# Kernel optimization log

Hardware: AMD Instinct MI355X
Metric: run time of the kernel (lower is better)

The kernel has to match this reference:

```python
import jax, jax.numpy as jnp
import numpy as np

N_NODES = 500000
N_EDGES = 16000000
IN_DIM = 17


def setup_inputs() -> dict:
    key = jax.random.key(0)
    k1, k2, k3, k4, k5, k6, k7 = jax.random.split(key, 7)
    x = jax.random.normal(k1, (N_NODES, IN_DIM), dtype=jnp.float32)
    edge_index = jax.random.randint(k2, (2, N_EDGES), 0, N_NODES, dtype=jnp.int64)
    edge_weight = jax.random.uniform(k3, (N_EDGES,), dtype=jnp.float32)
    # SAGEConv(17, 1): lin_l applied to aggregated neighbors (with bias),
    # lin_r applied to root features (no bias, PyG convention).
    s = 1.0 / np.sqrt(IN_DIM)
    w_l = jax.random.uniform(k4, (1, IN_DIM), minval=-s, maxval=s, dtype=jnp.float32)
    b_l = jax.random.uniform(k5, (1,), minval=-s, maxval=s, dtype=jnp.float32)
    w_r = jax.random.uniform(k6, (1, IN_DIM), minval=-s, maxval=s, dtype=jnp.float32)
    # out: Linear(1, 1)
    k8, k9 = jax.random.split(k7)
    w_o = jax.random.uniform(k8, (1, 1), minval=-1.0, maxval=1.0, dtype=jnp.float32)
    b_o = jax.random.uniform(k9, (1,), minval=-1.0, maxval=1.0, dtype=jnp.float32)
    return {"x": x, "edge_index": edge_index, "edge_weight": edge_weight,
            "w_l": w_l, "b_l": b_l, "w_r": w_r, "w_o": w_o, "b_o": b_o}


def reference(x, edge_index, edge_weight, w_l, b_l, w_r, w_o, b_o):
    # SAGEConv (mean aggregation). edge_weight is unused (faithful to PyG SAGEConv).
    # Project to out_dim=1 BEFORE aggregation (linearity makes this exact and
    # avoids materializing a [E,17] gathered buffer):
    #   lin_l(mean_j x_j) + b_l == mean_j (x_j @ W_l^T) + b_l
    src, dst = edge_index[0], edge_index[1]
    x_proj_l = x @ w_l.T                      # [N, 1]
    msg = x_proj_l[src, 0]                    # [E]  gathered source projections
    agg = jax.ops.segment_sum(msg, dst, num_segments=x.shape[0])          # [N]
    cnt = jax.ops.segment_sum(jnp.ones_like(msg), dst, num_segments=x.shape[0])
    mean = agg / jnp.maximum(cnt, 1.0)        # zero for isolated nodes
    h = mean[:, None] + b_l + x @ w_r.T       # [N, 1]  lin_l(aggr) + lin_r(x)
    h = jax.nn.elu(h)
    return h @ w_o.T + b_o                    # [N, 1]
```

## Files before the change

kernel.cpp:

```cpp
#include <hip/hip_runtime.h>
#include <hip/hip_bf16.h>
#include <math.h>

#define IN_DIM 17
#define NB 128
#define LOG_BN 12
#define BN 4096
#define K_SPLIT 16
#define CHUNK 8192
#define EPT 32
#define VAL_SCALE 4096.0f
#define FP_SCALE 268435456.0f
#define FP_INV   (1.0 / 268435456.0)

__global__ void node_proj_kernel(const float* __restrict__ x,
                                 const float* __restrict__ w_l,
                                 const float* __restrict__ w_r,
                                 float* __restrict__ p_l,
                                 float* __restrict__ p_r,
                                 int n_nodes) {
    int i = blockIdx.x * blockDim.x + threadIdx.x;
    if (i >= n_nodes) return;
    const float* row = x + (size_t)i * IN_DIM;
    float sl = 0.0f, sr = 0.0f;
#pragma unroll
    for (int k = 0; k < IN_DIM; ++k) {
        float v = row[k];
        sl = fmaf(v, w_l[k], sl);
        sr = fmaf(v, w_r[k], sr);
    }
    p_l[i] = sl;
    p_r[i] = sr;
}

__global__ __launch_bounds__(256, 4)
void sort_scatter_kernel(const int* __restrict__ src,
                         const int* __restrict__ dst,
                         const float* __restrict__ p_l,
                         unsigned* __restrict__ staging,
                         unsigned short* __restrict__ segtab,
                         int n_edges) {
    __shared__ unsigned hist[NB];
    __shared__ unsigned pos[NB];
    __shared__ unsigned sstart[NB + 1];
    __shared__ unsigned lbuf[CHUNK];

    const int tid = threadIdx.x;
    const int blk = blockIdx.x;
    const int e0 = blk * CHUNK;
    const int chunk_n = min(CHUNK, n_edges - e0);
    const int nvec = chunk_n >> 2;

    for (int t = tid; t < NB; t += 256) hist[t] = 0;
    __syncthreads();

    const uint4* dv = (const uint4*)(dst + e0);
    const uint4* sv = (const uint4*)(src + e0);
#pragma unroll
    for (int k = 0; k < EPT / 4; ++k) {
        int q = tid + k * 256;
        if (q < nvec) {
            uint4 d = dv[q];
            atomicAdd(&hist[d.x >> LOG_BN], 1u);
            atomicAdd(&hist[d.y >> LOG_BN], 1u);
            atomicAdd(&hist[d.z >> LOG_BN], 1u);
            atomicAdd(&hist[d.w >> LOG_BN], 1u);
        }
    }
    for (int i = (nvec << 2) + tid; i < chunk_n; i += 256)
        atomicAdd(&hist[(unsigned)dst[e0 + i] >> LOG_BN], 1u);
    __syncthreads();

    if (tid < 64) {
        unsigned c0 = hist[tid], c1 = hist[tid + 64];
        unsigned s0 = c0;
#pragma unroll
        for (int off = 1; off < 64; off <<= 1) {
            unsigned v = __shfl_up(s0, off);
            if (tid >= off) s0 += v;
        }
        unsigned tot0 = __shfl(s0, 63);
        unsigned s1 = c1;
#pragma unroll
        for (int off = 1; off < 64; off <<= 1) {
            unsigned v = __shfl_up(s1, off);
            if (tid >= off) s1 += v;
        }
        s1 += tot0;
        sstart[tid + 1] = s0;
        sstart[tid + 65] = s1;
        if (tid == 0) sstart[0] = 0;
        pos[tid] = (tid == 0) ? 0u : 0u;
    }
    __syncthreads();
    for (int t = tid; t < NB; t += 256) pos[t] = sstart[t];
    __syncthreads();

    for (int t = tid; t <= NB; t += 256)
        segtab[(size_t)blk * (NB + 2) + t] = (unsigned short)sstart[t];

#pragma unroll
    for (int k = 0; k < EPT / 4; ++k) {
        int q = tid + k * 256;
        if (q < nvec) {
            uint4 d = dv[q];
            uint4 s = sv[q];
            float pf[4] = {p_l[s.x], p_l[s.y], p_l[s.z], p_l[s.w]};
            unsigned dd[4] = {d.x, d.y, d.z, d.w};
#pragma unroll
            for (int u = 0; u < 4; ++u) {
                int fx = __float2int_rn(pf[u] * VAL_SCALE);
                fx = max(-32768, min(32767, fx));
                unsigned entry = ((unsigned)(fx & 0xFFFF) << 16) | (dd[u] & (BN - 1));
                unsigned b = dd[u] >> LOG_BN;
                unsigned p = atomicAdd(&pos[b], 1u);
                lbuf[p] = entry;
            }
        }
    }
    for (int i = (nvec << 2) + tid; i < chunk_n; i += 256) {
        unsigned s = (unsigned)src[e0 + i];
        unsigned d = (unsigned)dst[e0 + i];
        int fx = __float2int_rn(p_l[s] * VAL_SCALE);
        fx = max(-32768, min(32767, fx));
        unsigned entry = ((unsigned)(fx & 0xFFFF) << 16) | (d & (BN - 1));
        unsigned b = d >> LOG_BN;
        unsigned p = atomicAdd(&pos[b], 1u);
        lbuf[p] = entry;
    }
    __syncthreads();

    uint4* outp = (uint4*)(staging + (size_t)blk * CHUNK);
    const uint4* lp = (const uint4*)lbuf;
    int nv4 = (chunk_n + 3) >> 2;
    for (int q = tid; q < nv4; q += 256)
        outp[q] = lp[q];
}

__global__ __launch_bounds__(256, 8)
void reduce_kernel(const unsigned* __restrict__ staging,
                   const unsigned short* __restrict__ segtab,
                   unsigned* __restrict__ partials,
                   int nblk) {
    __shared__ unsigned lds_p[BN];
    const int tid = threadIdx.x;
    const int b = blockIdx.x / K_SPLIT;
    const int j = blockIdx.x % K_SPLIT;
    const int wave = tid >> 6, lane = tid & 63;

    for (int i = tid; i < BN; i += 256) lds_p[i] = 0u;
    __syncthreads();

    const int blk0 = (int)((long long)nblk * j / K_SPLIT);
    const int blk1 = (int)((long long)nblk * (j + 1) / K_SPLIT);

    int blk = blk0 + wave;
    unsigned s_nxt = 0, e_nxt = 0;
    if (blk < blk1) {
        const unsigned short* st = segtab + (size_t)blk * (NB + 2) + b;
        s_nxt = st[0];
        e_nxt = st[1];
    }
    while (blk < blk1) {
        unsigned s = s_nxt, e = e_nxt;
        const int nxt = blk + 4;
        if (nxt < blk1) {
            const unsigned short* st = segtab + (size_t)nxt * (NB + 2) + b;
            s_nxt = st[0];
            e_nxt = st[1];
        }
        const unsigned* sp = staging + (size_t)blk * CHUNK;
        for (unsigned i = s + lane; i < e; i += 64) {
            unsigned en = sp[i];
            int v = (int)(short)(en >> 16);
            atomicAdd(&lds_p[en & (BN - 1)], ((unsigned)v << 8) | 1u);
        }
        blk = nxt;
    }
    __syncthreads();
    size_t out_base = (size_t)blockIdx.x * BN;
    for (int i = tid; i < BN; i += 256)
        partials[out_base + i] = lds_p[i];
}

__global__ void finalize_kernel(const float* __restrict__ p_r,
                                const unsigned* __restrict__ partials,
                                const float* __restrict__ b_l,
                                const float* __restrict__ w_o,
                                const float* __restrict__ b_o,
                                float* __restrict__ out,
                                int n_nodes) {
    int i = blockIdx.x * blockDim.x + threadIdx.x;
    if (i >= n_nodes) return;
    int b = i >> LOG_BN;
    int loc = i & (BN - 1);
    int sum24 = 0, cnt = 0;
#pragma unroll
    for (int j = 0; j < K_SPLIT; ++j) {
        unsigned u = partials[((size_t)b * K_SPLIT + j) * BN + loc];
        sum24 += ((int)u) >> 8;
        cnt += (int)(u & 0xFFu);
    }
    float sum = (float)sum24 * (1.0f / VAL_SCALE);
    float mean = sum / fmaxf((float)cnt, 1.0f);
    float h = mean + b_l[0] + p_r[i];
    h = (h > 0.0f) ? h : expm1f(h);
    out[i] = fmaf(h, w_o[0], b_o[0]);
}

__global__ void edge_scatter_fb(const int* __restrict__ edge_index,
                                const float* __restrict__ p_l,
                                unsigned long long* __restrict__ bins,
                                int n_edges) {
    int e = blockIdx.x * blockDim.x + threadIdx.x;
    if (e >= n_edges) return;
    int s = edge_index[e];
    int d = edge_index[n_edges + e];
    float p = p_l[s];
    long long sfx = (long long)llrintf(p * FP_SCALE);
    unsigned long long delta = ((unsigned long long)sfx << 20) | 1ULL;
    atomicAdd(&bins[d], delta);
}

__global__ void finalize_fb(const float* __restrict__ p_r,
                            const unsigned long long* __restrict__ bins,
                            const float* __restrict__ b_l,
                            const float* __restrict__ w_o,
                            const float* __restrict__ b_o,
                            float* __restrict__ out,
                            int n_nodes) {
    int i = blockIdx.x * blockDim.x + threadIdx.x;
    if (i >= n_nodes) return;
    long long packed = (long long)bins[i];
    int cntv = (int)(packed & 0xFFFFFLL);
    long long sfx = packed >> 20;
    float sum = (float)((double)sfx * FP_INV);
    float mean = sum / fmaxf((float)cntv, 1.0f);
    float h = mean + b_l[0] + p_r[i];
    h = (h > 0.0f) ? h : expm1f(h);
    out[i] = fmaf(h, w_o[0], b_o[0]);
}

static inline size_t align_up(size_t v, size_t a) { return (v + a - 1) & ~(a - 1); }

extern "C" void kernel_launch(void* const* d_in, const int* in_sizes, int n_in,
                              void* d_out, int out_size, void* d_ws, size_t ws_size,
                              hipStream_t stream) {
    const float* x   = (const float*)d_in[0];
    const int*   ei  = (const int*)d_in[1];
    const float* w_l = (const float*)d_in[3];
    const float* b_l = (const float*)d_in[4];
    const float* w_r = (const float*)d_in[5];
    const float* w_o = (const float*)d_in[6];
    const float* b_o = (const float*)d_in[7];
    float* out = (float*)d_out;

    const int n_nodes = in_sizes[0] / IN_DIM;
    const int n_edges = in_sizes[2];
    const int* src = ei;
    const int* dst = ei + n_edges;
    const int nblk = (n_edges + CHUNK - 1) / CHUNK;

    char* ws = (char*)d_ws;
    size_t off = 0;
    size_t o_pl = off;      off = align_up(off + (size_t)n_nodes * 4, 256);
    size_t o_pr = off;      off = align_up(off + (size_t)n_nodes * 4, 256);
    size_t o_stage = off;   off = align_up(off + (size_t)nblk * CHUNK * 4, 256);
    size_t o_seg = off;     off = align_up(off + (size_t)nblk * (NB + 2) * 2, 256);
    size_t o_part = off;    off = align_up(off + (size_t)NB * K_SPLIT * BN * 4, 256);
    size_t need = off;

    float* p_l = (float*)(ws + o_pl);
    float* p_r = (float*)(ws + o_pr);

    const int B = 256;
    node_proj_kernel<<<(n_nodes + B - 1) / B, B, 0, stream>>>(x, w_l, w_r, p_l, p_r, n_nodes);

    if (ws_size >= need) {
        unsigned* staging       = (unsigned*)(ws + o_stage);
        unsigned short* segtab  = (unsigned short*)(ws + o_seg);
        unsigned* partials      = (unsigned*)(ws + o_part);

        sort_scatter_kernel<<<nblk, B, 0, stream>>>(src, dst, p_l, staging, segtab, n_edges);
        reduce_kernel<<<NB * K_SPLIT, B, 0, stream>>>(staging, segtab, partials, nblk);
        finalize_kernel<<<(n_nodes + B - 1) / B, B, 0, stream>>>(p_r, partials, b_l, w_o, b_o,
                                                                 out, n_nodes);
    } else {
        unsigned long long* bins = (unsigned long long*)(ws + o_stage);
        hipMemsetAsync(bins, 0, (size_t)n_nodes * 8, stream);
        edge_scatter_fb<<<(n_edges + B - 1) / B, B, 0, stream>>>(ei, p_l, bins, n_edges);
        finalize_fb<<<(n_nodes + B - 1) / B, B, 0, stream>>>(p_r, bins, b_l, w_o, b_o,
                                                             out, n_nodes);
    }
}
```

Measured before the change: 356.5 us.

## Halve sort chunk size and merge reduce partials via global atomics

The sort chunk drops from 8192 to 4096 edges per block, and occupancy is raised so more blocks run per CU. The reduce kernel now splits each wave into two half-waves that process separate chunks, since the per-bucket segments per chunk are short. Instead of writing K_SPLIT partial tables that finalize must re-read, each reduce block atomically adds its LDS bins into one zeroed global bin table, which needs an extra memset. Smaller chunks double the segment-table overhead, and the packed counts in the low 8 bits now hold the full per-node total rather than per-split partials, so nodes with high in-degree could overflow.

```diff
diff --git a/kernel.cpp b/kernel.cpp
--- a/kernel.cpp
+++ b/kernel.cpp
@@ -7,8 +7,8 @@
 #define LOG_BN 12
 #define BN 4096
 #define K_SPLIT 16
-#define CHUNK 8192
-#define EPT 32
+#define CHUNK 4096
+#define EPT 16
 #define VAL_SCALE 4096.0f
 #define FP_SCALE 268435456.0f
 #define FP_INV   (1.0 / 268435456.0)
@@ -33,7 +33,7 @@
     p_r[i] = sr;
 }
 
-__global__ __launch_bounds__(256, 4)
+__global__ __launch_bounds__(256, 8)
 void sort_scatter_kernel(const int* __restrict__ src,
                          const int* __restrict__ dst,
                          const float* __restrict__ p_l,
@@ -90,7 +90,6 @@
         sstart[tid + 1] = s0;
         sstart[tid + 65] = s1;
         if (tid == 0) sstart[0] = 0;
-        pos[tid] = (tid == 0) ? 0u : 0u;
     }
     __syncthreads();
     for (int t = tid; t < NB; t += 256) pos[t] = sstart[t];
@@ -140,13 +139,15 @@
 __global__ __launch_bounds__(256, 8)
 void reduce_kernel(const unsigned* __restrict__ staging,
                    const unsigned short* __restrict__ segtab,
-                   unsigned* __restrict__ partials,
+                   unsigned* __restrict__ bins,
                    int nblk) {
     __shared__ unsigned lds_p[BN];
     const int tid = threadIdx.x;
     const int b = blockIdx.x / K_SPLIT;
     const int j = blockIdx.x % K_SPLIT;
-    const int wave = tid >> 6, lane = tid & 63;
+    const int wave = tid >> 6;
+    const int half = (tid >> 5) & 1;
+    const int lane32 = tid & 31;
 
     for (int i = tid; i < BN; i += 256) lds_p[i] = 0u;
     __syncthreads();
@@ -154,37 +155,43 @@
     const int blk0 = (int)((long long)nblk * j / K_SPLIT);
     const int blk1 = (int)((long long)nblk * (j + 1) / K_SPLIT);
 
-    int blk = blk0 + wave;
+    int cur = blk0 + wave * 2 + half;
     unsigned s_nxt = 0, e_nxt = 0;
-    if (blk < blk1) {
-        const unsigned short* st = segtab + (size_t)blk * (NB + 2) + b;
+    if (cur < blk1) {
+        const unsigned short* st = segtab + (size_t)cur * (NB + 2) + b;
         s_nxt = st[0];
         e_nxt = st[1];
     }
-    while (blk < blk1) {
+    for (int base = blk0 + wave * 2; base < blk1; base += 8) {
+        const int myblk = base + half;
         unsigned s = s_nxt, e = e_nxt;
-        const int nxt = blk + 4;
+        const int nxt = myblk + 8;
         if (nxt < blk1) {
             const unsigned short* st = segtab + (size_t)nxt * (NB + 2) + b;
             s_nxt = st[0];
             e_nxt = st[1];
-        }
-        const unsigned* sp = staging + (size_t)blk * CHUNK;
-        for (unsigned i = s + lane; i < e; i += 64) {
-            unsigned en = sp[i];
-            int v = (int)(short)(en >> 16);
-            atomicAdd(&lds_p[en & (BN - 1)], ((unsigned)v << 8) | 1u);
-        }
-        blk = nxt;
-    }
-    __syncthreads();
-    size_t out_base = (size_t)blockIdx.x * BN;
-    for (int i = tid; i < BN; i += 256)
-        partials[out_base + i] = lds_p[i];
+        } else {
+            s_nxt = 0; e_nxt = 0;
+        }
+        if (myblk < blk1) {
+            const unsigned* sp = staging + (size_t)myblk * CHUNK;
+            for (unsigned i = s + lane32; i < e; i += 32) {
+                unsigned en = sp[i];
+                int v = (int)(short)(en >> 16);
+                atomicAdd(&lds_p[en & (BN - 1)], ((unsigned)v << 8) | 1u);
+            }
+        }
+    }
+    __syncthreads();
+    unsigned* gb = bins + (size_t)b * BN;
+    for (int i = tid; i < BN; i += 256) {
+        unsigned v = lds_p[i];
+        if (v) atomicAdd(&gb[i], v);
+    }
 }
 
 __global__ void finalize_kernel(const float* __restrict__ p_r,
-                                const unsigned* __restrict__ partials,
+                                const unsigned* __restrict__ bins,
                                 const float* __restrict__ b_l,
                                 const float* __restrict__ w_o,
                                 const float* __restrict__ b_o,
@@ -192,15 +199,9 @@
                                 int n_nodes) {
     int i = blockIdx.x * blockDim.x + threadIdx.x;
     if (i >= n_nodes) return;
-    int b = i >> LOG_BN;
-    int loc = i & (BN - 1);
-    int sum24 = 0, cnt = 0;
-#pragma unroll
-    for (int j = 0; j < K_SPLIT; ++j) {
-        unsigned u = partials[((size_t)b * K_SPLIT + j) * BN + loc];
-        sum24 += ((int)u) >> 8;
-        cnt += (int)(u & 0xFFu);
-    }
+    unsigned u = bins[i];
+    int sum24 = ((int)u) >> 8;
+    int cnt = (int)(u & 0xFFu);
     float sum = (float)sum24 * (1.0f / VAL_SCALE);
     float mean = sum / fmaxf((float)cnt, 1.0f);
     float h = mean + b_l[0] + p_r[i];
@@ -267,7 +268,7 @@
     size_t o_pr = off;      off = align_up(off + (size_t)n_nodes * 4, 256);
     size_t o_stage = off;   off = align_up(off + (size_t)nblk * CHUNK * 4, 256);
     size_t o_seg = off;     off = align_up(off + (size_t)nblk * (NB + 2) * 2, 256);
-    size_t o_part = off;    off = align_up(off + (size_t)NB * K_SPLIT * BN * 4, 256);
+    size_t o_bins = off;    off = align_up(off + (size_t)NB * BN * 4, 256);
     size_t need = off;
 
     float* p_l = (float*)(ws + o_pl);
@@ -279,11 +280,12 @@
     if (ws_size >= need) {
         unsigned* staging       = (unsigned*)(ws + o_stage);
         unsigned short* segtab  = (unsigned short*)(ws + o_seg);
-        unsigned* partials      = (unsigned*)(ws + o_part);
-
+        unsigned* bins          = (unsigned*)(ws + o_bins);
+
+        hipMemsetAsync(bins, 0, (size_t)NB * BN * 4, stream);
         sort_scatter_kernel<<<nblk, B, 0, stream>>>(src, dst, p_l, staging, segtab, n_edges);
-        reduce_kernel<<<NB * K_SPLIT, B, 0, stream>>>(staging, segtab, partials, nblk);
-        finalize_kernel<<<(n_nodes + B - 1) / B, B, 0, stream>>>(p_r, partials, b_l, w_o, b_o,
+        reduce_kernel<<<NB * K_SPLIT, B, 0, stream>>>(staging, segtab, bins, nblk);
+        finalize_kernel<<<(n_nodes + B - 1) / B, B, 0, stream>>>(p_r, bins, b_l, w_o, b_o,
                                                                  out, n_nodes);
     } else {
         unsigned long long* bins = (unsigned long long*)(ws + o_stage);
```

New measurement: 363.7 us. 2.0% more time.
